# Kernel tuning notes

Hardware: AMD Instinct MI355X
Metric: run time of the kernel (lower is better)

The kernel has to match this reference:

```python
import jax, jax.numpy as jnp
import numpy as np

D_MODEL = 1024
D_Q = 1024
D_K = 1024
D_V = 1024
B, S = 4, 2048


def setup_inputs() -> dict:
    key = jax.random.key(0)
    kx, kq, kk, kv = jax.random.split(key, 4)
    # torch Linear(in, out) weight is [out, in]; y = x @ W.T. Use kaiming-ish scale.
    sc = 1.0 / np.sqrt(D_MODEL)
    x = jax.random.normal(kx, (B, S, D_MODEL), dtype=jnp.float32)
    Wq = jax.random.normal(kq, (D_Q, D_MODEL), dtype=jnp.float32) * sc
    Wk = jax.random.normal(kk, (D_K, D_MODEL), dtype=jnp.float32) * sc
    Wv = jax.random.normal(kv, (D_V, D_MODEL), dtype=jnp.float32) * sc
    return {"x": x, "Wq": Wq, "Wk": Wk, "Wv": Wv}


def reference(x, Wq, Wk, Wv):
    d_k = Wk.shape[0]
    q = jnp.einsum('bsd,qd->bsq', x, Wq)  # [B,S,d_q]
    k = jnp.einsum('bsd,kd->bsk', x, Wk)  # [B,S,d_k]
    v = jnp.einsum('bsd,vd->bsv', x, Wv)  # [B,S,d_v]
    scores = jnp.einsum('bqd,bkd->bqk', q, k) / jnp.sqrt(jnp.float32(d_k))
    seq = scores.shape[-1]
    causal = jnp.tril(jnp.ones((seq, seq), dtype=bool))  # True = keep
    scores = jnp.where(causal[None, :, :], scores, -jnp.inf)
    probs = jax.nn.softmax(scores, axis=-1)
    return jnp.einsum('bqk,bkv->bqv', probs, v)
```

## Files before the change

kernel.cpp:

```cpp
#include <hip/hip_runtime.h>
#include <hip/hip_bf16.h>
#include <stdint.h>

typedef __attribute__((ext_vector_type(8))) short short8;
typedef __attribute__((ext_vector_type(4))) float floatx4;

typedef const __attribute__((address_space(1))) void* gvp;
typedef __attribute__((address_space(3))) void* lvp;

__device__ __forceinline__ unsigned short f2bf(float f) {
    unsigned u = __float_as_uint(f);
    u += 0x7fffu + ((u >> 16) & 1u);
    return (unsigned short)(u >> 16);
}

#define BAR()    do { asm volatile("" ::: "memory"); __builtin_amdgcn_s_barrier(); asm volatile("" ::: "memory"); } while (0)
#define WAITL()  do { asm volatile("s_waitcnt lgkmcnt(0)" ::: "memory"); __builtin_amdgcn_sched_barrier(0); } while (0)
#define WAITV4() asm volatile("s_waitcnt vmcnt(4)" ::: "memory")
#define WAITV0() asm volatile("s_waitcnt vmcnt(0)" ::: "memory")

__global__ __launch_bounds__(256)
void cvt_all(const float* __restrict__ x, const float* __restrict__ wq,
             const float* __restrict__ wk, const float* __restrict__ wv,
             unsigned short* __restrict__ Xb, unsigned short* __restrict__ WqT,
             unsigned short* __restrict__ WkT, unsigned short* __restrict__ Wvb) {
    const int b = blockIdx.x, t = threadIdx.x;
    if (b < 2304) {
        const float* in; unsigned short* out; long base;
        if (b < 2048) { in = x;  out = Xb;  base = (long)b * 1024; }
        else          { in = wv; out = Wvb; base = (long)(b - 2048) * 1024; }
        #pragma unroll
        for (int k = 0; k < 4; ++k) {
            long idx = base + k * 256 + t;
            float4 v = reinterpret_cast<const float4*>(in)[idx];
            uint2 o;
            o.x = (unsigned)f2bf(v.x) | ((unsigned)f2bf(v.y) << 16);
            o.y = (unsigned)f2bf(v.z) | ((unsigned)f2bf(v.w) << 16);
            reinterpret_cast<uint2*>(out)[idx] = o;
        }
    } else {
        const int bb = b - 2304;
        const float* in = (bb < 256) ? wq : wk;
        unsigned short* out = (bb < 256) ? WqT : WkT;
        const int tile = bb & 255;
        const int e0 = (tile >> 4) * 64, d0 = (tile & 15) * 64;
        __shared__ unsigned short ldsT[64][68];
        const int r = t >> 4, cq = t & 15;
        #pragma unroll
        for (int p = 0; p < 4; ++p) {
            const int e = p * 16 + r;
            float4 v = *reinterpret_cast<const float4*>(in + (long)(e0 + e) * 1024 + d0 + cq * 4);
            ldsT[cq*4+0][e] = f2bf(v.x);
            ldsT[cq*4+1][e] = f2bf(v.y);
            ldsT[cq*4+2][e] = f2bf(v.z);
            ldsT[cq*4+3][e] = f2bf(v.w);
        }
        __syncthreads();
        #pragma unroll
        for (int p = 0; p < 4; ++p) {
            const int d = p * 16 + r;
            ushort4 o = *reinterpret_cast<const ushort4*>(&ldsT[d][cq * 4]);
            *reinterpret_cast<ushort4*>(out + (long)(d0 + d) * 1024 + e0 + cq * 4) = o;
        }
    }
}

__device__ __forceinline__ void stage_tile(unsigned short* Abuf, unsigned short* Bbuf,
                                           const unsigned short* A, int lda,
                                           const unsigned short* B, int ldb, int k0,
                                           int wid, int srow, int piece) {
    #pragma unroll
    for (int i = 0; i < 4; ++i) {
        const int c = wid * 4 + i;
        const int row = c * 8 + srow;
        const int cs = (piece * 16) ^ ((row & 7) << 4);
        __builtin_amdgcn_global_load_lds(
            (gvp)(reinterpret_cast<const char*>(A + (long)row * lda + k0) + cs),
            (lvp)(reinterpret_cast<char*>(Abuf) + c * 1024), 16, 0, 0);
        __builtin_amdgcn_global_load_lds(
            (gvp)(reinterpret_cast<const char*>(B + (long)row * ldb + k0) + cs),
            (lvp)(reinterpret_cast<char*>(Bbuf) + c * 1024), 16, 0, 0);
    }
}

__device__ __forceinline__ void compute_tile(floatx4 acc[4][4], const unsigned short* As,
                                             const unsigned short* Bs, int wm, int wn,
                                             int frow, int lane) {
    #pragma unroll
    for (int ks = 0; ks < 2; ++ks) {
        short8 af[4], bf[4];
        const int colb = ks * 64 + (lane >> 4) * 16;
        #pragma unroll
        for (int i = 0; i < 4; ++i) {
            const int ar = wm + i * 16 + frow;
            af[i] = *reinterpret_cast<const short8*>(
                reinterpret_cast<const char*>(As) + ar * 128 + (colb ^ ((ar & 7) << 4)));
            const int br = wn + i * 16 + frow;
            bf[i] = *reinterpret_cast<const short8*>(
                reinterpret_cast<const char*>(Bs) + br * 128 + (colb ^ ((br & 7) << 4)));
        }
        #pragma unroll
        for (int i = 0; i < 4; ++i)
            #pragma unroll
            for (int j = 0; j < 4; ++j)
                acc[i][j] = __builtin_amdgcn_mfma_f32_16x16x32_bf16(af[i], bf[j], acc[i][j], 0, 0, 0);
    }
}

__global__ __launch_bounds__(256, 2)
void g_chunk(const unsigned short* __restrict__ WkT, const unsigned short* __restrict__ WqT,
             float* __restrict__ Gw) {
    const int bx = blockIdx.x, by = blockIdx.y, bz = blockIdx.z;
    const unsigned short* A = WkT + (long)by * 128 * 1024;
    const unsigned short* B = WqT + (long)bx * 128 * 1024;

    __shared__ unsigned short As[2][128 * 64];
    __shared__ unsigned short Bs[2][128 * 64];

    const int tid = threadIdx.x, lane = tid & 63, wid = tid >> 6;
    const int srow = lane >> 3, piece = lane & 7;
    const int wm = (wid >> 1) * 64, wn = (wid & 1) * 64, frow = lane & 15;

    floatx4 acc[4][4] = {};
    const int kbase = bz * 256;

    stage_tile(As[0], Bs[0], A, 1024, B, 1024, kbase, wid, srow, piece);
    WAITV0(); BAR();
    int cur = 0;
    #pragma unroll 1
    for (int t = 0; t < 4; ++t) {
        if (t < 3)
            stage_tile(As[cur ^ 1], Bs[cur ^ 1], A, 1024, B, 1024, kbase + (t + 1) * 64,
                       wid, srow, piece);
        compute_tile(acc, As[cur], Bs[cur], wm, wn, frow, lane);
        WAITV0(); BAR();
        cur ^= 1;
    }

    float* Cb = Gw + (long)bz * (1 << 20) + (long)(by * 128) * 1024 + bx * 128;
    const int cr0 = wm + (lane >> 4) * 4;
    const int cc0 = wn + (lane & 15);
    #pragma unroll
    for (int i = 0; i < 4; ++i)
        #pragma unroll
        for (int j = 0; j < 4; ++j)
            #pragma unroll
            for (int r = 0; r < 4; ++r)
                Cb[(long)(cr0 + i * 16 + r) * 1024 + cc0 + j * 16] = acc[i][j][r];
}

__global__ __launch_bounds__(256)
void reduce_g(const float* __restrict__ Gw, unsigned short* __restrict__ Gp) {
    const long i4 = (long)blockIdx.x * 256 + threadIdx.x;
    const long M4 = (1l << 20) / 4;
    float4 a = reinterpret_cast<const float4*>(Gw)[i4];
    float4 b = reinterpret_cast<const float4*>(Gw)[i4 + M4];
    float4 c = reinterpret_cast<const float4*>(Gw)[i4 + 2 * M4];
    float4 d = reinterpret_cast<const float4*>(Gw)[i4 + 3 * M4];
    float sx = (a.x + b.x + c.x + d.x) * 0.03125f;
    float sy = (a.y + b.y + c.y + d.y) * 0.03125f;
    float sz = (a.z + b.z + c.z + d.z) * 0.03125f;
    float sw = (a.w + b.w + c.w + d.w) * 0.03125f;
    uint2 o;
    o.x = (unsigned)f2bf(sx) | ((unsigned)f2bf(sy) << 16);
    o.y = (unsigned)f2bf(sz) | ((unsigned)f2bf(sw) << 16);
    reinterpret_cast<uint2*>(Gp)[i4] = o;
}

__global__ __launch_bounds__(256, 2)
void pv_pair(const unsigned short* __restrict__ P, const unsigned short* __restrict__ Vt,
             float* __restrict__ out) {
    const int flat = (blockIdx.z * 8 + blockIdx.y) * 8 + blockIdx.x;
    const int xcd = flat & 7, lid = flat >> 3;
    const int bz = xcd >> 1;
    const int bx = (xcd & 1) * 4 + (lid & 3);
    const int pj = lid >> 2;

    const unsigned short* Pb = P + (long)bz * 2048 * 4096;
    const unsigned short* Bv = Vt + (long)bz * 1024 * 2048 + (long)(bx * 128) * 2048;
    float* Cb = out + (long)bz * 2048 * 1024;

    __shared__ unsigned short As[2][128 * 64];
    __shared__ unsigned short Bs[2][128 * 64];

    const int tid = threadIdx.x, lane = tid & 63, wid = tid >> 6;
    const int srow = lane >> 3, piece = lane & 7;
    const int wm = (wid >> 1) * 64, wn = (wid & 1) * 64, frow = lane & 15;

    #pragma unroll 1
    for (int j = 0; j < 2; ++j) {
        const int by = j ? 15 - pj : pj;
        const unsigned short* A = Pb + (long)by * 128 * 4096;
        const int nt = (by + 1) * 2;

        floatx4 acc[4][4] = {};
        stage_tile(As[0], Bs[0], A, 4096, Bv, 2048, 0, wid, srow, piece);
        WAITV0(); BAR();
        int cur = 0;
        #pragma unroll 1
        for (int t = 0; t < nt; ++t) {
            if (t + 1 < nt)
                stage_tile(As[cur ^ 1], Bs[cur ^ 1], A, 4096, Bv, 2048, (t + 1) * 64,
                           wid, srow, piece);
            compute_tile(acc, As[cur], Bs[cur], wm, wn, frow, lane);
            WAITV0(); BAR();
            cur ^= 1;
        }

        float* Cj = Cb + (long)(by * 128) * 1024 + bx * 128;
        const int cr0 = wm + (lane >> 4) * 4;
        const int cc0 = wn + (lane & 15);
        #pragma unroll
        for (int i = 0; i < 4; ++i)
            #pragma unroll
            for (int jj = 0; jj < 4; ++jj)
                #pragma unroll
                for (int r = 0; r < 4; ++r)
                    Cj[(long)(cr0 + i * 16 + r) * 1024 + cc0 + jj * 16] = acc[i][jj][r];
    }
}

__device__ __forceinline__ void stage_half(char* slot, const unsigned short* src,
                                           int ld, int k0, int tid) {
    #pragma unroll
    for (int r = 0; r < 2; ++r) {
        const int c = r * 512 + tid;
        const int row = c >> 3;
        const int cs = ((c & 7) * 16) ^ ((row & 7) << 4);
        const char* g = reinterpret_cast<const char*>(src + (long)row * ld + k0) + cs;
        __builtin_amdgcn_global_load_lds((gvp)g,
            (lvp)(slot + r * 8192 + (tid >> 6) * 1024), 16, 0, 0);
    }
}

__device__ __forceinline__ void load_a4(short8 a_[4][2], const char* slot, int mh,
                                        int fr, int csw0, int csw1) {
    #pragma unroll
    for (int i = 0; i < 4; ++i) {
        const int rb = (mh * 64 + i * 16 + fr) * 128;
        a_[i][0] = *reinterpret_cast<const short8*>(slot + rb + csw0);
        a_[i][1] = *reinterpret_cast<const short8*>(slot + rb + csw1);
    }
}

__device__ __forceinline__ void load_b2(short8 b_[2][2], const char* slot, int rbase,
                                        int nh, int fr, int csw0, int csw1) {
    #pragma unroll
    for (int j = 0; j < 2; ++j) {
        const int rb = (rbase + nh * 32 + j * 16 + fr) * 128;
        b_[j][0] = *reinterpret_cast<const short8*>(slot + rb + csw0);
        b_[j][1] = *reinterpret_cast<const short8*>(slot + rb + csw1);
    }
}

__device__ __forceinline__ void mfma16(floatx4 acc[8][4], short8 a_[4][2],
                                       short8 b_[2][2], int mh, int nh) {
    __builtin_amdgcn_s_setprio(1);
    #pragma unroll
    for (int i = 0; i < 4; ++i)
        #pragma unroll
        for (int j = 0; j < 2; ++j) {
            acc[mh*4+i][nh*2+j] = __builtin_amdgcn_mfma_f32_16x16x32_bf16(
                a_[i][0], b_[j][0], acc[mh*4+i][nh*2+j], 0, 0, 0);
            acc[mh*4+i][nh*2+j] = __builtin_amdgcn_mfma_f32_16x16x32_bf16(
                a_[i][1], b_[j][1], acc[mh*4+i][nh*2+j], 0, 0, 0);
        }
    __builtin_amdgcn_s_setprio(0);
}

template<typename CT, int MODE>
__global__ __launch_bounds__(512, 2)
void gemm8p(const unsigned short* __restrict__ A, const unsigned short* B,
            const unsigned short* B1, CT* __restrict__ C, unsigned short* __restrict__ Vt,
            int K, int lda, int ldb, int ldc,
            long sA, long sB, long sC, int nwg)
{
    const int gx = gridDim.x, gy = gridDim.y;
    int flat = (blockIdx.z * gy + blockIdx.y) * gx + blockIdx.x;
    int bx, by, bz = 0;
    bool isV = false;
    if (MODE == 1) {
        int xcd = flat & 7, lid = flat >> 3;
        int q = nwg >> 3, r = nwg & 7;
        flat = (xcd < r ? xcd * (q + 1) : r * (q + 1) + (xcd - r) * q) + lid;
        bx = flat % gx;
        int t2 = flat / gx;
        by = t2 % gy;
        bz = t2 / gy;
        if (bx > by) return;
    } else {
        const int xcd = flat & 7, lid = flat >> 3;
        by = xcd + ((lid >> 3) << 3);
        const int sub = lid & 7;
        isV = (sub >> 2) != 0;
        bx = sub & 3;
        if (isV) B = B1;
    }

    A += (long)bz * sA + (long)by * 256 * lda;
    B += (long)bz * sB + (long)bx * 256 * ldb;
    C += (long)bz * sC;

    __shared__ __align__(16) char lds[8 * 16384];
    #define SLOT(db, op, half) (lds + ((((db) << 1 | (op)) << 1 | (half)) * 16384))

    const int tid  = threadIdx.x;
    const int lane = tid & 63;
    const int wid  = tid >> 6;
    const int wm = wid >> 2;
    const int wn = wid & 3;
    const int bh = wn >> 1;
    const int brbase = (wn & 1) * 64;
    const int fr = lane & 15;
    const int csw0 = ((lane >> 4) * 16) ^ ((fr & 7) << 4);
    const int csw1 = (64 + (lane >> 4) * 16) ^ ((fr & 7) << 4);

    const unsigned short* Ah[2] = { A, A + 128ll * lda };
    const unsigned short* Bh[2] = { B, B + 128ll * ldb };

    const int NT = K >> 6;
    const int NI = NT >> 1;

    floatx4 acc[8][4] = {};
    short8 a_[4][2];
    short8 b_[2][2][2];

    stage_half(SLOT(0,1,0), Bh[0], ldb, 0, tid);
    stage_half(SLOT(0,1,1), Bh[1], ldb, 0, tid);
    stage_half(SLOT(0,0,0), Ah[0], lda, 0, tid);
    stage_half(SLOT(0,0,1), Ah[1], lda, 0, tid);
    stage_half(SLOT(1,1,0), Bh[0], ldb, 64, tid);
    stage_half(SLOT(1,1,1), Bh[1], ldb, 64, tid);
    WAITV4();
    BAR();

    for (int I = 0; I < NI; ++I) {
        const int kA1 = min(2*I + 1, NT - 1) * 64;
        const int kT2 = min(2*I + 2, NT - 1) * 64;
        const int kB3 = min(2*I + 3, NT - 1) * 64;

        load_a4(a_, SLOT(0,0,wm), 0, fr, csw0, csw1);
        load_b2(b_[0], SLOT(0,1,bh), brbase, 0, fr, csw0, csw1);
        stage_half(SLOT(1,0,0), Ah[0], lda, kA1, tid);
        BAR(); WAITL();
        mfma16(acc, a_, b_[0], 0, 0);
        BAR();

        load_b2(b_[1], SLOT(0,1,bh), brbase, 1, fr, csw0, csw1);
        stage_half(SLOT(1,0,1), Ah[1], lda, kA1, tid);
        BAR(); WAITL();
        mfma16(acc, a_, b_[1], 0, 1);
        BAR();

        load_a4(a_, SLOT(0,0,wm), 1, fr, csw0, csw1);
        stage_half(SLOT(0,1,0), Bh[0], ldb, kT2, tid);
        BAR(); WAITL();
        mfma16(acc, a_, b_[1], 1, 1);
        BAR();

        stage_half(SLOT(0,1,1), Bh[1], ldb, kT2, tid);
        BAR(); WAITL();
        mfma16(acc, a_, b_[0], 1, 0);
        WAITV4();
        BAR();

        load_a4(a_, SLOT(1,0,wm), 0, fr, csw0, csw1);
        load_b2(b_[0], SLOT(1,1,bh), brbase, 0, fr, csw0, csw1);
        stage_half(SLOT(0,0,0), Ah[0], lda, kT2, tid);
        BAR(); WAITL();
        mfma16(acc, a_, b_[0], 0, 0);
        BAR();

        load_b2(b_[1], SLOT(1,1,bh), brbase, 1, fr, csw0, csw1);
        stage_half(SLOT(0,0,1), Ah[1], lda, kT2, tid);
        BAR(); WAITL();
        mfma16(acc, a_, b_[1], 0, 1);
        BAR();

        load_a4(a_, SLOT(1,0,wm), 1, fr, csw0, csw1);
        stage_half(SLOT(1,1,0), Bh[0], ldb, kB3, tid);
        BAR(); WAITL();
        mfma16(acc, a_, b_[1], 1, 1);
        BAR();

        stage_half(SLOT(1,1,1), Bh[1], ldb, kB3, tid);
        BAR(); WAITL();
        mfma16(acc, a_, b_[0], 1, 0);
        WAITV4();
        BAR();
    }

    if (MODE == 3 && isV) {
        WAITV0();
        BAR();
        char* T = lds;
        #pragma unroll
        for (int i = 0; i < 8; ++i)
            #pragma unroll
            for (int j = 0; j < 4; ++j) {
                const int n = wn * 64 + j * 16 + fr;
                const int m = wm * 128 + ((lane >> 4) << 2) + i * 16;
                uint2 pk;
                pk.x = (unsigned)f2bf(acc[i][j][0]) | ((unsigned)f2bf(acc[i][j][1]) << 16);
                pk.y = (unsigned)f2bf(acc[i][j][2]) | ((unsigned)f2bf(acc[i][j][3]) << 16);
                *reinterpret_cast<uint2*>(T + n * 512 + ((m * 2) ^ ((n & 7) << 4))) = pk;
            }
        __syncthreads();
        const int b  = by >> 3;
        const int s0 = (by & 7) * 256;
        #pragma unroll
        for (int c = 0; c < 16; ++c) {
            const int idx = c * 512 + tid;
            const int n = idx >> 5, k = idx & 31;
            uint4 v = *reinterpret_cast<const uint4*>(T + n * 512 + ((k * 16) ^ ((n & 7) << 4)));
            *reinterpret_cast<uint4*>(Vt + (long)b * (1024 * 2048)
                + (long)(bx * 256 + n) * 2048 + s0 + k * 8) = v;
        }
        return;
    }

    const int cr0 = by * 256 + wm * 128 + (lane >> 4) * 4;
    const int cc0 = bx * 256 + wn * 64 + (lane & 15);
    #pragma unroll
    for (int i = 0; i < 8; ++i)
        #pragma unroll
        for (int j = 0; j < 4; ++j)
            #pragma unroll
            for (int r = 0; r < 4; ++r) {
                long idx = (long)(cr0 + i * 16 + r) * ldc + (cc0 + j * 16);
                float v = acc[i][j][r];
                if constexpr (sizeof(CT) == 4) C[idx] = v;
                else                           C[idx] = (CT)f2bf(v);
            }
    #undef SLOT
}

__global__ __launch_bounds__(256)
void softmax_causal(float* __restrict__ Sc) {
    const int b = blockIdx.y;
    const int t = threadIdx.x;
    const int lane = t & 63, wid = t >> 6;
    __shared__ float rmax[2][4], rsum[2][4];

    #pragma unroll 1
    for (int h = 0; h < 2; ++h) {
        const int q = h ? 2047 - blockIdx.x : blockIdx.x;
        float* row = Sc + ((long)b * 2048 + q) * 2048;
        const int kend = (q | 127) + 1;

        float vals[8];
        float mx = -INFINITY;
        #pragma unroll
        for (int i = 0; i < 2; ++i) {
            const int c0 = i * 1024 + t * 4;
            if (c0 <= q) {
                float4 v = *reinterpret_cast<const float4*>(row + c0);
                float tmp[4] = {v.x, v.y, v.z, v.w};
                #pragma unroll
                for (int j = 0; j < 4; ++j) {
                    float val = (c0 + j <= q) ? tmp[j] : -INFINITY;
                    vals[i * 4 + j] = val;
                    mx = fmaxf(mx, val);
                }
            } else {
                vals[i*4+0] = vals[i*4+1] = vals[i*4+2] = vals[i*4+3] = -INFINITY;
            }
        }
        #pragma unroll
        for (int o = 32; o > 0; o >>= 1) mx = fmaxf(mx, __shfl_xor(mx, o));
        if (lane == 0) rmax[h][wid] = mx;
        __syncthreads();
        mx = fmaxf(fmaxf(rmax[h][0], rmax[h][1]), fmaxf(rmax[h][2], rmax[h][3]));

        float s = 0.f;
        #pragma unroll
        for (int k = 0; k < 8; ++k) {
            float e = __expf(vals[k] - mx);
            vals[k] = e;
            s += e;
        }
        #pragma unroll
        for (int o = 32; o > 0; o >>= 1) s += __shfl_xor(s, o);
        if (lane == 0) rsum[h][wid] = s;
        __syncthreads();
        s = rsum[h][0] + rsum[h][1] + rsum[h][2] + rsum[h][3];
        const float inv = 1.f / s;

        unsigned short* orow = reinterpret_cast<unsigned short*>(row);
        #pragma unroll
        for (int i = 0; i < 2; ++i) {
            const int c0 = i * 1024 + t * 4;
            if (c0 < kend) {
                uint2 o;
                o.x = (unsigned)f2bf(vals[i*4+0] * inv) | ((unsigned)f2bf(vals[i*4+1] * inv) << 16);
                o.y = (unsigned)f2bf(vals[i*4+2] * inv) | ((unsigned)f2bf(vals[i*4+3] * inv) << 16);
                *reinterpret_cast<uint2*>(orow + c0) = o;
            }
        }
    }
}

extern "C" void kernel_launch(void* const* d_in, const int* in_sizes, int n_in,
                              void* d_out, int out_size, void* d_ws, size_t ws_size,
                              hipStream_t stream) {
    const float* x  = (const float*)d_in[0];
    const float* Wq = (const float*)d_in[1];
    const float* Wk = (const float*)d_in[2];
    const float* Wv = (const float*)d_in[3];
    float* out = (float*)d_out;

    char* w = (char*)d_ws;
    unsigned short* Xb  = (unsigned short*)(w);
    unsigned short* WqT = (unsigned short*)(w + (16ll << 20));
    unsigned short* WkT = (unsigned short*)(w + (18ll << 20));
    unsigned short* Wvb = (unsigned short*)(w + (20ll << 20));
    unsigned short* Yb  = (unsigned short*)(w + (22ll << 20));
    unsigned short* Gp  = (unsigned short*)(w + (38ll << 20));
    float*          Gw  = (float*)(w + (40ll << 20));
    unsigned short* Vt  = (unsigned short*)(w + (70ll << 20));
    float* Sc = (float*)(w + (86ll << 20));

    dim3 blk(256);
    cvt_all<<<2816, blk, 0, stream>>>(x, Wq, Wk, Wv, Xb, WqT, WkT, Wvb);

    g_chunk<<<dim3(8, 8, 4), blk, 0, stream>>>(WkT, WqT, Gw);
    reduce_g<<<1024, blk, 0, stream>>>(Gw, Gp);

    gemm8p<unsigned short, 3><<<dim3(256, 1, 1), dim3(512), 0, stream>>>(
        Xb, Gp, Wvb, Yb, Vt, 1024, 1024, 1024, 1024,
        0, 0, 0, 256);

    gemm8p<float, 1><<<dim3(8, 8, 4), dim3(512), 0, stream>>>(
        Yb, Xb, nullptr, Sc, nullptr, 1024, 1024, 1024, 2048,
        2048ll * 1024, 2048ll * 1024, 2048ll * 2048, 256);

    softmax_causal<<<dim3(1024, 4), blk, 0, stream>>>(Sc);

    pv_pair<<<dim3(8, 8, 4), blk, 0, stream>>>((const unsigned short*)Sc, Vt, out);
}
```

Measured before the change: 143.7 us.

## Replace PV double buffer with 4-deep ring of K=32 subtiles

Result: no change. 140.9 us (-1.9%).

```diff
diff --git a/kernel.cpp b/kernel.cpp
--- a/kernel.cpp
+++ b/kernel.cpp
@@ -16,8 +16,10 @@
 
 #define BAR()    do { asm volatile("" ::: "memory"); __builtin_amdgcn_s_barrier(); asm volatile("" ::: "memory"); } while (0)
 #define WAITL()  do { asm volatile("s_waitcnt lgkmcnt(0)" ::: "memory"); __builtin_amdgcn_sched_barrier(0); } while (0)
-#define WAITV4() asm volatile("s_waitcnt vmcnt(4)" ::: "memory")
-#define WAITV0() asm volatile("s_waitcnt vmcnt(0)" ::: "memory")
+#define WAITV12() asm volatile("s_waitcnt vmcnt(12)")
+#define WAITV8()  asm volatile("s_waitcnt vmcnt(8)")
+#define WAITV4()  asm volatile("s_waitcnt vmcnt(4)")
+#define WAITV0()  asm volatile("s_waitcnt vmcnt(0)")
 
 __global__ __launch_bounds__(256)
 void cvt_all(const float* __restrict__ x, const float* __restrict__ wq,
@@ -167,44 +169,91 @@
     reinterpret_cast<uint2*>(Gp)[i4] = o;
 }
 
+__device__ __forceinline__ void stage_sub(char* Aslot, char* Bslot,
+                                          const unsigned short* A, int lda,
+                                          const unsigned short* B, int ldb, int k0,
+                                          int wid, int lane) {
+    const int r  = lane >> 2;
+    const int pg = (lane & 3) ^ (r & 3) ^ ((r >> 2) & 3);
+    #pragma unroll
+    for (int i = 0; i < 2; ++i) {
+        const int chunk = wid * 2 + i;
+        const int row = chunk * 16 + r;
+        __builtin_amdgcn_global_load_lds(
+            (gvp)(A + (long)row * lda + k0 + pg * 8),
+            (lvp)(Aslot + chunk * 1024), 16, 0, 0);
+        __builtin_amdgcn_global_load_lds(
+            (gvp)(B + (long)row * ldb + k0 + pg * 8),
+            (lvp)(Bslot + chunk * 1024), 16, 0, 0);
+    }
+}
+
+__device__ __forceinline__ void compute_sub(floatx4 acc[4][4], const char* Asl,
+                                            const char* Bsl, int wm, int wn,
+                                            int frow, int lane) {
+    short8 af[4], bf[4];
+    const int cp = lane >> 4;
+    #pragma unroll
+    for (int i = 0; i < 4; ++i) {
+        const int ar = wm + i * 16 + frow;
+        af[i] = *reinterpret_cast<const short8*>(
+            Asl + ar * 64 + ((cp ^ (ar & 3) ^ ((ar >> 2) & 3)) << 4));
+        const int br = wn + i * 16 + frow;
+        bf[i] = *reinterpret_cast<const short8*>(
+            Bsl + br * 64 + ((cp ^ (br & 3) ^ ((br >> 2) & 3)) << 4));
+    }
+    WAITL();
+    __builtin_amdgcn_s_setprio(1);
+    #pragma unroll
+    for (int i = 0; i < 4; ++i)
+        #pragma unroll
+        for (int j = 0; j < 4; ++j)
+            acc[i][j] = __builtin_amdgcn_mfma_f32_16x16x32_bf16(af[i], bf[j], acc[i][j], 0, 0, 0);
+    __builtin_amdgcn_s_setprio(0);
+}
+
 __global__ __launch_bounds__(256, 2)
-void pv_pair(const unsigned short* __restrict__ P, const unsigned short* __restrict__ Vt,
+void pv_ring(const unsigned short* __restrict__ P, const unsigned short* __restrict__ Vt,
              float* __restrict__ out) {
-    const int flat = (blockIdx.z * 8 + blockIdx.y) * 8 + blockIdx.x;
-    const int xcd = flat & 7, lid = flat >> 3;
-    const int bz = xcd >> 1;
-    const int bx = (xcd & 1) * 4 + (lid & 3);
-    const int pj = lid >> 2;
+    int flat = (blockIdx.z * 8 + blockIdx.y) * 8 + blockIdx.x;
+    { int xcd = flat & 7, lid = flat >> 3; flat = xcd * 32 + lid; }
+    const int bx = flat % 8;
+    const int pj = (flat / 8) % 8;
+    const int bz = flat / 64;
 
     const unsigned short* Pb = P + (long)bz * 2048 * 4096;
     const unsigned short* Bv = Vt + (long)bz * 1024 * 2048 + (long)(bx * 128) * 2048;
     float* Cb = out + (long)bz * 2048 * 1024;
 
-    __shared__ unsigned short As[2][128 * 64];
-    __shared__ unsigned short Bs[2][128 * 64];
+    __shared__ __align__(16) char ring[4][2][8192];
 
     const int tid = threadIdx.x, lane = tid & 63, wid = tid >> 6;
-    const int srow = lane >> 3, piece = lane & 7;
     const int wm = (wid >> 1) * 64, wn = (wid & 1) * 64, frow = lane & 15;
 
     #pragma unroll 1
     for (int j = 0; j < 2; ++j) {
         const int by = j ? 15 - pj : pj;
         const unsigned short* A = Pb + (long)by * 128 * 4096;
-        const int nt = (by + 1) * 2;
+        const int NS = (by + 1) * 4;
 
         floatx4 acc[4][4] = {};
-        stage_tile(As[0], Bs[0], A, 4096, Bv, 2048, 0, wid, srow, piece);
-        WAITV0(); BAR();
-        int cur = 0;
+        stage_sub(ring[0][0], ring[0][1], A, 4096, Bv, 2048, 0,  wid, lane);
+        stage_sub(ring[1][0], ring[1][1], A, 4096, Bv, 2048, 32, wid, lane);
+        stage_sub(ring[2][0], ring[2][1], A, 4096, Bv, 2048, 64, wid, lane);
+
         #pragma unroll 1
-        for (int t = 0; t < nt; ++t) {
-            if (t + 1 < nt)
-                stage_tile(As[cur ^ 1], Bs[cur ^ 1], A, 4096, Bv, 2048, (t + 1) * 64,
-                           wid, srow, piece);
-            compute_tile(acc, As[cur], Bs[cur], wm, wn, frow, lane);
-            WAITV0(); BAR();
-            cur ^= 1;
+        for (int p = 0; p < NS; ++p) {
+            BAR();
+            if (p + 3 < NS)
+                stage_sub(ring[(p + 3) & 3][0], ring[(p + 3) & 3][1],
+                          A, 4096, Bv, 2048, (p + 3) * 32, wid, lane);
+            const int rem = min(NS - 1, p + 3) - p;
+            if (rem >= 3)      { WAITV12(); }
+            else if (rem == 2) { WAITV8();  }
+            else if (rem == 1) { WAITV4();  }
+            else               { WAITV0();  }
+            BAR();
+            compute_sub(acc, ring[p & 3][0], ring[p & 3][1], wm, wn, frow, lane);
         }
 
         float* Cj = Cb + (long)(by * 128) * 1024 + bx * 128;
@@ -217,6 +266,9 @@
                 #pragma unroll
                 for (int r = 0; r < 4; ++r)
                     Cj[(long)(cr0 + i * 16 + r) * 1024 + cc0 + jj * 16] = acc[i][jj][r];
+
+        WAITV0();
+        BAR();
     }
 }
 
@@ -267,6 +319,8 @@
         }
     __builtin_amdgcn_s_setprio(0);
 }
+
+#define WAITV4G() asm volatile("s_waitcnt vmcnt(4)")
 
 template<typename CT, int MODE>
 __global__ __launch_bounds__(512, 2)
@@ -331,7 +385,7 @@
     stage_half(SLOT(0,0,1), Ah[1], lda, 0, tid);
     stage_half(SLOT(1,1,0), Bh[0], ldb, 64, tid);
     stage_half(SLOT(1,1,1), Bh[1], ldb, 64, tid);
-    WAITV4();
+    WAITV4G();
     BAR();
 
     for (int I = 0; I < NI; ++I) {
@@ -361,7 +415,7 @@
         stage_half(SLOT(0,1,1), Bh[1], ldb, kT2, tid);
         BAR(); WAITL();
         mfma16(acc, a_, b_[0], 1, 0);
-        WAITV4();
+        WAITV4G();
         BAR();
 
         load_a4(a_, SLOT(1,0,wm), 0, fr, csw0, csw1);
@@ -386,7 +440,7 @@
         stage_half(SLOT(1,1,1), Bh[1], ldb, kB3, tid);
         BAR(); WAITL();
         mfma16(acc, a_, b_[0], 1, 0);
-        WAITV4();
+        WAITV4G();
         BAR();
     }
 
@@ -536,5 +590,5 @@
 
     softmax_causal<<<dim3(1024, 4), blk, 0, stream>>>(Sc);
 
-    pv_pair<<<dim3(8, 8, 4), blk, 0, stream>>>((const unsigned short*)Sc, Vt, out);
-}
+    pv_ring<<<dim3(8, 8, 4), blk, 0, stream>>>((const unsigned short*)Sc, Vt, out);
+}
```
